# Kernel optimization log

Hardware: AMD Instinct MI355X
Metric: run time of the kernel (lower is better)

The kernel has to match this reference:

```python
import jax, jax.numpy as jnp
import numpy as np

B, T, D = 32, 200, 256
H, DH = 4, 32
INNER = H * DH  # 128
L, FF, NI = 8, 1024, 100000
NB = 64  # gap/recency buckets


def _ln(x, g, b, eps=1e-5):
    m = x.mean(-1, keepdims=True)
    v = jnp.mean((x - m) ** 2, -1, keepdims=True)
    return (x - m) / jnp.sqrt(v + eps) * g + b


def _gelu(x):
    return jax.nn.gelu(x, approximate=False)


def _dwconv_causal(x, w, b):
    # x: [B,T,C], w: [C,k] depthwise kernel, causal left-pad (k-1)
    k = w.shape[1]
    xp = jnp.pad(x, ((0, 0), (k - 1, 0), (0, 0))).transpose(0, 2, 1)  # [B,C,T+k-1]
    out = jax.lax.conv_general_dilated(
        xp, w[:, None, :], (1,), 'VALID',
        dimension_numbers=('NCH', 'OIH', 'NCH'), feature_group_count=w.shape[0])
    return out.transpose(0, 2, 1) + b


def _causal_linear_attention(q, k, v, m4):
    q = (jax.nn.elu(q) + 1.0) * m4
    k = (jax.nn.elu(k) + 1.0) * m4
    v = v * m4
    kv = jnp.einsum('bthd,bthe->bthde', k, v)          # [B,T,H,DH,DH]
    kv_prefix = jnp.cumsum(kv, axis=1)
    k_prefix = jnp.cumsum(k, axis=1)
    num = jnp.einsum('bthd,bthde->bthe', q, kv_prefix)
    den = jnp.sum(q * k_prefix, -1, keepdims=True)
    return num / (den + 1e-6) * m4


def _forward(item_emb, pos_emb, gap_emb, rec_emb, tf_w1, tf_b1, tf_w2, tf_b2,
             in_g, in_b, l_ln1g, l_ln1b, l_win, l_bin, l_wc, l_bc, l_tw, l_tb,
             l_pw, l_pb, l_wmix, l_bmix, l_ln2g, l_ln2b, l_wf1, l_bf1, l_wf2, l_bf2,
             fn_g, fn_b, pg_w, pg_b, uh_w1, uh_b1, uh_lng, uh_lnb, uh_w2, uh_b2,
             item_bias, ids, ts, lens):
    Bb, Tt = ids.shape
    pos = jnp.arange(Tt)
    mask = pos[None, :] >= (Tt - lens)[:, None]  # right-aligned valid mask [B,T]
    prev_ts = jnp.roll(ts, 1, axis=1)
    prev_mask = jnp.roll(mask, 1, axis=1).at[:, 0].set(False)
    zero = jnp.zeros_like(ts)
    gap_vals = jnp.where(mask & prev_mask, jnp.maximum(ts - prev_ts, 0), zero)
    latest = ts[:, -1:]
    rec_vals = jnp.where(mask, jnp.maximum(latest - ts, 0), zero)

    def buck(v, n):
        vf = jnp.maximum(v.astype(jnp.float32), 0.0)
        return jnp.clip(jnp.floor(jnp.log2(vf + 1.0)), 0, n - 1).astype(jnp.int32)

    gb = buck(gap_vals, NB)
    rb = buck(rec_vals, NB)
    rec_raw = jnp.maximum(latest - ts, 0).astype(jnp.float32)
    tf = jnp.stack([jnp.log1p(gb.astype(jnp.float32)), jnp.log1p(rec_raw)], -1)  # [B,T,2]
    dense_time = _gelu(tf @ tf_w1 + tf_b1) @ tf_w2 + tf_b2

    x = item_emb[ids] + pos_emb[None] + gap_emb[gb] + rec_emb[rb] + dense_time
    mf = mask[..., None].astype(x.dtype)
    m4 = mask[..., None, None].astype(x.dtype)
    x = _ln(x, in_g, in_b) * mf

    for i in range(L):
        res = x
        nrm = _ln(x, l_ln1g[i], l_ln1b[i])
        proj = nrm @ l_win[i] + l_bin[i]  # [B,T,D+3*INNER]
        gate = proj[..., :D]
        q = proj[..., D:D + INNER].reshape(Bb, Tt, H, DH)
        k = proj[..., D + INNER:D + 2 * INNER].reshape(Bb, Tt, H, DH)
        v = proj[..., D + 2 * INNER:].reshape(Bb, Tt, H, DH)
        content = _causal_linear_attention(q, k, v, m4).reshape(Bb, Tt, INNER) @ l_wc[i] + l_bc[i]
        temporal = _dwconv_causal(nrm, l_tw[i], l_tb[i])
        positional = _dwconv_causal(nrm, l_pw[i], l_pb[i])
        mixed = jnp.concatenate([content, temporal, positional], -1) @ l_wmix[i] + l_bmix[i]
        x = (res + jax.nn.sigmoid(gate) * mixed) * mf
        h = _ln(x, l_ln2g[i], l_ln2b[i])
        ffn = _gelu(h @ l_wf1[i] + l_bf1[i]) @ l_wf2[i] + l_bf2[i]
        x = (x + ffn) * mf

    x = _ln(x, fn_g, fn_b) * mf
    denom = jnp.maximum(lens, 1)[:, None].astype(x.dtype)
    mean_pooled = (x * mf).sum(1) / denom
    ps = (x @ pg_w + pg_b)[..., 0]
    ps = jnp.where(mask, ps, -1e9)
    pw = jax.nn.softmax(ps, axis=1)[..., None]
    attn_pooled = (pw * x).sum(1)
    last = x[:, -1, :]
    u = jnp.concatenate([last, mean_pooled, attn_pooled], -1)
    u = _gelu(u @ uh_w1 + uh_b1)
    u = _ln(u, uh_lng, uh_lnb)
    u = u @ uh_w2 + uh_b2
    u = u / jnp.maximum(jnp.linalg.norm(u, axis=-1, keepdims=True), 1e-12)
    ie = item_emb[1:]
    ie = ie / jnp.maximum(jnp.linalg.norm(ie, axis=-1, keepdims=True), 1e-12)
    return u @ ie.T + item_bias[1:]


def setup_inputs() -> dict:
    key = jax.random.key(0)
    it = iter(jax.random.split(key, 64))
    def nk():
        return next(it)
    def w(*s):
        return jax.random.normal(nk(), s, jnp.float32) * 0.02
    inp = dict(
        history_ids=jax.random.randint(nk(), (B, T), 0, NI),
        history_timestamps=jnp.sort(jax.random.randint(nk(), (B, T), 0, 1000000), axis=1),
        history_lengths=jax.random.randint(nk(), (B,), 1, T + 1),
        item_emb=w(NI + 1, D).at[0].set(0.0),
        pos_emb=w(T, D), gap_emb=w(NB, D), rec_emb=w(NB, D),
        tf_w1=w(2, D), tf_b1=jnp.zeros((D,)), tf_w2=w(D, D), tf_b2=jnp.zeros((D,)),
        in_g=jnp.ones((D,)), in_b=jnp.zeros((D,)),
        l_ln1g=jnp.ones((L, D)), l_ln1b=jnp.zeros((L, D)),
        l_win=w(L, D, D + 3 * INNER), l_bin=jnp.zeros((L, D + 3 * INNER)),
        l_wc=w(L, INNER, D), l_bc=jnp.zeros((L, D)),
        l_tw=w(L, D, 3), l_tb=jnp.zeros((L, D)),
        l_pw=w(L, D, 5), l_pb=jnp.zeros((L, D)),
        l_wmix=w(L, 3 * D, D), l_bmix=jnp.zeros((L, D)),
        l_ln2g=jnp.ones((L, D)), l_ln2b=jnp.zeros((L, D)),
        l_wf1=w(L, D, FF), l_bf1=jnp.zeros((L, FF)),
        l_wf2=w(L, FF, D), l_bf2=jnp.zeros((L, D)),
        fn_g=jnp.ones((D,)), fn_b=jnp.zeros((D,)),
        pg_w=w(D, 1), pg_b=jnp.zeros((1,)),
        uh_w1=w(3 * D, 1024), uh_b1=jnp.zeros((1024,)),
        uh_lng=jnp.ones((1024,)), uh_lnb=jnp.zeros((1024,)),
        uh_w2=w(1024, D), uh_b2=jnp.zeros((D,)),
        item_bias=jnp.zeros((NI + 1,)),
    )
    return inp


def reference(history_ids, history_timestamps, history_lengths, item_emb, pos_emb,
              gap_emb, rec_emb, tf_w1, tf_b1, tf_w2, tf_b2, in_g, in_b, l_ln1g,
              l_ln1b, l_win, l_bin, l_wc, l_bc, l_tw, l_tb, l_pw, l_pb, l_wmix,
              l_bmix, l_ln2g, l_ln2b, l_wf1, l_bf1, l_wf2, l_bf2, fn_g, fn_b,
              pg_w, pg_b, uh_w1, uh_b1, uh_lng, uh_lnb, uh_w2, uh_b2, item_bias):
    return _forward(item_emb, pos_emb, gap_emb, rec_emb, tf_w1, tf_b1, tf_w2, tf_b2,
                    in_g, in_b, l_ln1g, l_ln1b, l_win, l_bin, l_wc, l_bc, l_tw, l_tb,
                    l_pw, l_pb, l_wmix, l_bmix, l_ln2g, l_ln2b, l_wf1, l_bf1, l_wf2,
                    l_bf2, fn_g, fn_b, pg_w, pg_b, uh_w1, uh_b1, uh_lng, uh_lnb,
                    uh_w2, uh_b2, item_bias, history_ids, history_timestamps,
                    history_lengths)
```

## Files before the change

kernel.cpp:

```cpp
#include <hip/hip_runtime.h>
#include <math.h>

#define B_ 32
#define T_ 200
#define D_ 256
#define H_ 4
#define DH_ 32
#define INNER_ 128
#define L_ 8
#define FF_ 1024
#define NI_ 100000
#define NB_ 64
#define CH_ 25

typedef __attribute__((ext_vector_type(8))) short short8;
typedef __attribute__((ext_vector_type(8))) unsigned short ushort8;
typedef __attribute__((ext_vector_type(4))) unsigned short ushort4v;
typedef __attribute__((ext_vector_type(4))) float floatx4;

__device__ __forceinline__ float gelu_f(float x){
  return 0.5f*x*(1.0f+erff(x*0.70710678118654752f));
}
__device__ __forceinline__ float wsum(float v){
  #pragma unroll
  for (int o=32;o>0;o>>=1) v += __shfl_xor(v,o,64);
  return v;
}
__device__ __forceinline__ unsigned short f2bf(float x){
  unsigned int u = __float_as_uint(x);
  unsigned int r = (u + 0x7fffu + ((u>>16)&1u)) >> 16;
  return (unsigned short)r;
}
__device__ __forceinline__ float bf2f(unsigned short u){
  return __uint_as_float(((unsigned int)u)<<16);
}

__device__ __forceinline__ void cvt_tile(const float* __restrict__ src, unsigned short* __restrict__ dst,
                                         int K, int N, int tk, int tn, int tid, float (*s)[33])
{
  int tx = tid & 31, ty0 = tid >> 5;
  #pragma unroll
  for (int it=0; it<4; ++it){
    int ty = ty0 + it*8;
    s[ty][tx] = src[(size_t)(tk*32+ty)*N + tn*32+tx];
  }
  __syncthreads();
  #pragma unroll
  for (int it=0; it<4; ++it){
    int ty = ty0 + it*8;
    dst[(size_t)(tn*32+ty)*K + tk*32 + tx] = f2bf(s[tx][ty]);
  }
}

__global__ __launch_bounds__(256) void k_cvtAll(
  const float* __restrict__ win, const float* __restrict__ wmix,
  const float* __restrict__ wf1, const float* __restrict__ wf2,
  const float* __restrict__ tfw2, const float* __restrict__ uhw1, const float* __restrict__ uhw2,
  unsigned short* __restrict__ WtPerm, unsigned short* __restrict__ WtMixT,
  unsigned short* __restrict__ WtH)
{
  __shared__ float s[32][33];
  int b = blockIdx.x, tid = threadIdx.x;
  if (b < 6912){
    int l = b / 864, r = b % 864;
    if (r < 160)      cvt_tile(win + (size_t)l*163840, WtPerm + (size_t)l*688128,          256, 640,  r/20,      r%20,      tid, s);
    else if (r < 352){int t=r-160; cvt_tile(wmix + (size_t)l*196608, WtMixT + (size_t)l*196608, 768, 256, t/8, t%8, tid, s);}
    else if (r < 608){int t=r-352; cvt_tile(wf1 + (size_t)l*262144, WtPerm + (size_t)l*688128 + 163840, 256, 1024, t/32, t%32, tid, s);}
    else             {int t=r-608; cvt_tile(wf2 + (size_t)l*262144, WtPerm + (size_t)l*688128 + 425984, 1024, 256, t/8, t%8, tid, s);}
  } else {
    int r = b - 6912;
    if (r < 64)       cvt_tile(tfw2, WtH,        256, 256,  r/8,  r%8,  tid, s);
    else if (r < 832){int t=r-64;  cvt_tile(uhw1, WtH+65536,  768, 1024, t/32, t%32, tid, s);}
    else             {int t=r-832; cvt_tile(uhw2, WtH+851968, 1024, 256, t/8,  t%8,  tid, s);}
  }
}

__global__ __launch_bounds__(256) void k_asm(
  const float* __restrict__ WcombF, const unsigned short* __restrict__ WtMixT,
  unsigned short* __restrict__ WtBig)
{
  int l = blockIdx.x >> 3, g = blockIdx.x & 7;
  int tid = threadIdx.x;
  int n = g*32 + (tid >> 3);
  int k0 = (tid & 7) * 80;
  const float* wc = WcombF + (size_t)l*32768;
  const unsigned short* wm = WtMixT + (size_t)l*196608 + (size_t)n*768;
  unsigned short* dst = WtBig + (size_t)l*163840 + (size_t)n*640;
  for (int kk=0; kk<80; kk++){
    int k = k0 + kk;
    dst[k] = (k < 128) ? f2bf(wc[(size_t)k*256 + n]) : wm[k+128];
  }
}

__global__ __launch_bounds__(256) void k_bfold(
  const float* __restrict__ bc, const float* __restrict__ bmix,
  const float* __restrict__ wmix, float* __restrict__ bmixP)
{
  int l = blockIdx.x; int n = threadIdx.x;
  const float* w = wmix + (size_t)l*196608;
  const float* c = bc + l*256;
  float s = bmix[l*256 + n];
  for (int d=0; d<256; d++) s += c[d]*w[(size_t)d*256 + n];
  bmixP[l*256+n] = s;
}

template<int TN>
__global__ __launch_bounds__(256) void k_gemm_bf(
    const float* __restrict__ A, const unsigned short* __restrict__ Wt,
    const float* __restrict__ bias, float* __restrict__ C,
    int M, int N, int K, int ldA, int ldW, int ldC, int mode,
    size_t sA, size_t sW, size_t sC, size_t sB)
{
  constexpr int NJ = TN/32;
  __shared__ unsigned short Als[128][40];
  __shared__ unsigned short Bls[TN][40];
  int z = blockIdx.z;
  A += (size_t)z*sA; Wt += (size_t)z*sW; C += (size_t)z*sC;
  const float* bz = bias ? bias + (size_t)z*sB : nullptr;
  int tid = threadIdx.x;
  int wave = tid >> 6, lane = tid & 63;
  int wm = (wave >> 1) * 64, wn = (wave & 1) * (TN/2);
  int frow = lane & 15, kg = lane >> 4;
  int bm = blockIdx.y * 128, bn = blockIdx.x * TN;
  int sm = tid >> 1, skh = (tid & 1) * 16;

  floatx4 acc[4][NJ];
  #pragma unroll
  for (int i=0;i<4;i++)
    #pragma unroll
    for (int j=0;j<NJ;j++) acc[i][j] = (floatx4){0.f,0.f,0.f,0.f};

  for (int k0=0; k0<K; k0+=32){
    {
      int gm = bm + sm;
      float f[16];
      if (gm < M){
        const float4* ap = (const float4*)(A + (size_t)gm*ldA + k0 + skh);
        #pragma unroll
        for (int c=0;c<4;c++){ float4 v = ap[c]; f[c*4]=v.x; f[c*4+1]=v.y; f[c*4+2]=v.z; f[c*4+3]=v.w; }
      } else {
        #pragma unroll
        for (int c=0;c<16;c++) f[c]=0.f;
      }
      ushort8 pa, pb;
      #pragma unroll
      for (int c=0;c<8;c++){ pa[c]=f2bf(f[c]); pb[c]=f2bf(f[8+c]); }
      *(ushort8*)&Als[sm][skh]   = pa;
      *(ushort8*)&Als[sm][skh+8] = pb;
    }
    #pragma unroll
    for (int u=0; u<TN/64; u++){
      int li = tid + u*256;
      int row = li >> 2, koff = (li & 3) * 8;
      int gn = bn + row;
      ushort8 wv;
      if (gn < N){
        wv = *(const ushort8*)&Wt[(size_t)gn*ldW + k0 + koff];
      } else {
        for (int c=0;c<8;c++) wv[c]=0;
      }
      *(ushort8*)&Bls[row][koff] = wv;
    }
    __syncthreads();
    short8 af[4], bf[NJ];
    #pragma unroll
    for (int i=0;i<4;i++) af[i] = *(const short8*)&Als[wm + 16*i + frow][kg*8];
    #pragma unroll
    for (int j=0;j<NJ;j++) bf[j] = *(const short8*)&Bls[wn + 16*j + frow][kg*8];
    #pragma unroll
    for (int i=0;i<4;i++)
      #pragma unroll
      for (int j=0;j<NJ;j++)
        acc[i][j] = __builtin_amdgcn_mfma_f32_16x16x32_bf16(af[i], bf[j], acc[i][j], 0, 0, 0);
    __syncthreads();
  }

  #pragma unroll
  for (int j=0;j<NJ;j++){
    int n = bn + wn + 16*j + frow;
    float bv = bz ? bz[n] : 0.f;
    #pragma unroll
    for (int i=0;i<4;i++){
      int m0 = bm + wm + 16*i + kg*4;
      #pragma unroll
      for (int r=0;r<4;r++){
        int m = m0 + r;
        if (m < M){
          float v = acc[i][j][r] + bv;
          if (mode == 1) v = gelu_f(v);
          float* cp = &C[(size_t)m*ldC + n];
          if (mode == 2) v += *cp;
          *cp = v;
        }
      }
    }
  }
}

__global__ __launch_bounds__(256) void k_gemm16(
    const unsigned short* __restrict__ A, const unsigned short* __restrict__ Wt,
    const float* __restrict__ bias, void* __restrict__ Cv,
    int K, int ldA, int ldW, int ldC, int mode)
{
  int tid = threadIdx.x;
  int wave = tid >> 6, lane = tid & 63;
  int frow = lane & 15, kg = lane >> 4;
  int bm = blockIdx.y * 32;
  int bn = blockIdx.x * 128 + wave * 32;

  const unsigned short* a0 = A + (size_t)(bm + frow)*ldA + kg*8;
  const unsigned short* a1 = a0 + (size_t)16*ldA;
  const unsigned short* b0 = Wt + (size_t)(bn + frow)*ldW + kg*8;
  const unsigned short* b1 = b0 + (size_t)16*ldW;

  floatx4 acc[2][2];
  #pragma unroll
  for (int i=0;i<2;i++)
    #pragma unroll
    for (int j=0;j<2;j++) acc[i][j] = (floatx4){0.f,0.f,0.f,0.f};

  #pragma unroll 4
  for (int k0=0; k0<K; k0+=32){
    short8 af0 = *(const short8*)(a0 + k0);
    short8 af1 = *(const short8*)(a1 + k0);
    short8 bf0 = *(const short8*)(b0 + k0);
    short8 bf1 = *(const short8*)(b1 + k0);
    acc[0][0] = __builtin_amdgcn_mfma_f32_16x16x32_bf16(af0, bf0, acc[0][0], 0, 0, 0);
    acc[0][1] = __builtin_amdgcn_mfma_f32_16x16x32_bf16(af0, bf1, acc[0][1], 0, 0, 0);
    acc[1][0] = __builtin_amdgcn_mfma_f32_16x16x32_bf16(af1, bf0, acc[1][0], 0, 0, 0);
    acc[1][1] = __builtin_amdgcn_mfma_f32_16x16x32_bf16(af1, bf1, acc[1][1], 0, 0, 0);
  }

  float* Cf = (float*)Cv;
  unsigned short* Ch = (unsigned short*)Cv;
  #pragma unroll
  for (int j=0;j<2;j++){
    int n = bn + 16*j + frow;
    float bv = bias[n];
    #pragma unroll
    for (int i=0;i<2;i++){
      int m0 = bm + 16*i + kg*4;
      #pragma unroll
      for (int r=0;r<4;r++){
        float v = acc[i][j][r] + bv;
        size_t off = (size_t)(m0+r)*ldC + n;
        if (mode == 1)      Cf[off] = gelu_f(v);
        else if (mode == 2) Cf[off] += v;
        else if (mode == 4) Ch[off] = f2bf(gelu_f(v));
        else                Cf[off] = v;
      }
    }
  }
}

__global__ __launch_bounds__(256) void k_embed(
  const int* __restrict__ ids, const int* __restrict__ ts, const int* __restrict__ lens,
  const float* __restrict__ item_emb, const float* __restrict__ pos_emb,
  const float* __restrict__ gap_emb, const float* __restrict__ rec_emb,
  const float* __restrict__ tf_w1, const float* __restrict__ tf_b1,
  float* __restrict__ xbuf, unsigned short* __restrict__ tfh)
{
  int bt = blockIdx.x;
  int b = bt / T_, t = bt % T_;
  int d = threadIdx.x;
  int len = lens[b];
  int tcur = ts[b*T_+t];
  int tlast = ts[b*T_+T_-1];
  bool mask  = t >= T_ - len;
  bool pmask = (t >= 1) && ((t-1) >= T_ - len);
  int gap = 0;
  if (mask && pmask){ int pv = ts[b*T_+t-1]; gap = max(tcur - pv, 0); }
  int rec = mask ? max(tlast - tcur, 0) : 0;
  int gb = min(max((int)floorf(log2f((float)gap + 1.0f)), 0), NB_-1);
  int rb = min(max((int)floorf(log2f((float)rec + 1.0f)), 0), NB_-1);
  float rec_raw = (float)max(tlast - tcur, 0);
  float tf0 = log1pf((float)gb);
  float tf1 = log1pf(rec_raw);
  float hid = gelu_f(tf0*tf_w1[d] + tf1*tf_w1[D_+d] + tf_b1[d]);
  tfh[(size_t)bt*D_ + d] = f2bf(hid);
  int id = ids[b*T_+t];
  xbuf[(size_t)bt*D_ + d] = item_emb[(size_t)id*D_ + d] + pos_emb[t*D_ + d]
                          + gap_emb[gb*D_ + d] + rec_emb[rb*D_ + d];
}

template<int NC>
__global__ __launch_bounds__(256) void k_ln(
  const float* __restrict__ in, void* __restrict__ out,
  const float* __restrict__ g, const float* __restrict__ bb,
  int rows, const int* __restrict__ lens, int applyMask, int outBf)
{
  int wid = threadIdx.x >> 6, lane = threadIdx.x & 63;
  int r = blockIdx.x*4 + wid;
  if (r >= rows) return;
  const int D = NC*256;
  const float4* rp = (const float4*)(in + (size_t)r*D);
  float4 v[NC];
  float s = 0.f;
  #pragma unroll
  for (int c=0;c<NC;c++){ v[c] = rp[c*64 + lane]; s += v[c].x+v[c].y+v[c].z+v[c].w; }
  s = wsum(s);
  float mean = s / (float)D;
  float q = 0.f;
  #pragma unroll
  for (int c=0;c<NC;c++){
    float a=v[c].x-mean, b2=v[c].y-mean, c2=v[c].z-mean, d2=v[c].w-mean;
    q += a*a + b2*b2 + c2*c2 + d2*d2;
  }
  q = wsum(q);
  float rstd = rsqrtf(q/(float)D + 1e-5f);
  float m = 1.f;
  if (applyMask){ int t = r % T_; int b = r / T_; m = (t >= T_ - lens[b]) ? 1.f : 0.f; }
  #pragma unroll
  for (int c=0;c<NC;c++){
    float4 gg  = ((const float4*)g )[c*64+lane];
    float4 bv  = ((const float4*)bb)[c*64+lane];
    float4 o;
    o.x = ((v[c].x-mean)*rstd*gg.x + bv.x)*m;
    o.y = ((v[c].y-mean)*rstd*gg.y + bv.y)*m;
    o.z = ((v[c].z-mean)*rstd*gg.z + bv.z)*m;
    o.w = ((v[c].w-mean)*rstd*gg.w + bv.w)*m;
    if (outBf){
      ushort4v ob; ob.x=f2bf(o.x); ob.y=f2bf(o.y); ob.z=f2bf(o.z); ob.w=f2bf(o.w);
      ((ushort4v*)((unsigned short*)out + (size_t)r*D))[c*64+lane] = ob;
    } else {
      ((float4*)((float*)out + (size_t)r*D))[c*64+lane] = o;
    }
  }
}

__global__ __launch_bounds__(64) void k_attn_sums(
  const float* __restrict__ proj, const int* __restrict__ lens, float* __restrict__ Ssum)
{
  int blk = blockIdx.x;
  int bh = blk >> 3, c = blk & 7;
  int b = bh >> 2, h = bh & 3;
  int lane = threadIdx.x; int e = lane & 31, half = lane >> 5;
  int tstart = T_ - lens[b];
  __shared__ float sk[CH_*32], sv[CH_*32];
  int t0 = c*CH_;
  for (int idx = lane; idx < CH_*32; idx += 64){
    int tl = idx >> 5, dd = idx & 31;
    int t = t0 + tl;
    float m = (t >= tstart) ? 1.f : 0.f;
    const float* pr = proj + (size_t)(b*T_+t)*640 + h*32 + dd;
    float kw = pr[384], vv = pr[512];
    sk[idx] = (kw > 0.f ? kw + 1.f : __expf(kw)) * m;
    sv[idx] = vv * m;
  }
  __syncthreads();
  float acc[16];
  #pragma unroll
  for (int j=0;j<16;j++) acc[j]=0.f;
  for (int tl=0; tl<CH_; tl++){
    const float4* k4 = (const float4*)(sk + tl*32 + half*16);
    float vf = sv[tl*32 + e];
    #pragma unroll
    for (int jj=0;jj<4;jj++){
      float4 kk = k4[jj];
      acc[jj*4+0] += kk.x*vf;
      acc[jj*4+1] += kk.y*vf;
      acc[jj*4+2] += kk.z*vf;
      acc[jj*4+3] += kk.w*vf;
    }
  }
  float* dst = Ssum + ((size_t)bh*8 + c)*1056;
  #pragma unroll
  for (int j=0;j<16;j++) dst[(half*16+j)*32 + e] = acc[j];
  if (half == 0){
    float s = 0.f;
    for (int tl=0; tl<CH_; tl++) s += sk[tl*32 + e];
    dst[1024 + e] = s;
  }
}

__global__ __launch_bounds__(64) void k_attn_out(
  const float* __restrict__ proj, const int* __restrict__ lens,
  const float* __restrict__ Ssum, unsigned short* __restrict__ cat)
{
  int blk = blockIdx.x;
  int bh = blk >> 3, c = blk & 7;
  int b = bh >> 2, h = bh & 3;
  int lane = threadIdx.x; int e = lane & 31, half = lane >> 5;
  int tstart = T_ - lens[b];
  __shared__ float sq[CH_*32], sk[CH_*32], sv[CH_*32];
  __shared__ float P[1056];
  __shared__ float A[CH_][CH_+1];
  __shared__ float sden[CH_];
  int t0 = c*CH_;
  const float* base = Ssum + (size_t)bh*8*1056;
  for (int idx = lane; idx < 1056; idx += 64){
    float s = 0.f;
    for (int cp=0; cp<c; cp++) s += base[cp*1056 + idx];
    P[idx] = s;
  }
  for (int idx = lane; idx < CH_*32; idx += 64){
    int tl = idx >> 5, dd = idx & 31;
    int t = t0 + tl;
    float m = (t >= tstart) ? 1.f : 0.f;
    const float* pr = proj + (size_t)(b*T_+t)*640 + h*32 + dd;
    float qv = pr[256], kw = pr[384], vv = pr[512];
    sq[idx] = (qv > 0.f ? qv + 1.f : __expf(qv)) * m;
    sk[idx] = (kw > 0.f ? kw + 1.f : __expf(kw)) * m;
    sv[idx] = vv * m;
  }
  __syncthreads();
  for (int idx = lane; idx < CH_*CH_; idx += 64){
    int t = idx / CH_, tp = idx - t*CH_;
    float s = 0.f;
    if (tp <= t){
      const float4* q4 = (const float4*)(sq + t*32);
      const float4* k4 = (const float4*)(sk + tp*32);
      #pragma unroll
      for (int jj=0;jj<8;jj++){
        float4 qq = q4[jj], kk = k4[jj];
        s += qq.x*kk.x + qq.y*kk.y + qq.z*kk.z + qq.w*kk.w;
      }
    }
    A[t][tp] = s;
  }
  __syncthreads();
  if (lane < CH_){
    int t = lane;
    float s = 0.f;
    for (int tp=0; tp<=t; tp++) s += A[t][tp];
    const float* qf = sq + t*32;
    #pragma unroll
    for (int d=0; d<32; d++) s += qf[d]*P[1024+d];
    sden[t] = s;
  }
  __syncthreads();
  int tlo = half ? 13 : 0;
  int thi = half ? CH_ : 13;
  for (int t = tlo; t < thi; t++){
    float num = 0.f;
    for (int tp=0; tp<=t; tp++) num += A[t][tp]*sv[tp*32+e];
    const float* qf = sq + t*32;
    #pragma unroll
    for (int d=0; d<32; d++) num += qf[d]*P[d*32+e];
    int tg = t0 + t;
    float m = (tg >= tstart) ? 1.f : 0.f;
    cat[(size_t)(b*T_+tg)*640 + h*32 + e] = f2bf(num/(sden[t]+1e-6f)*m);
  }
}

__global__ __launch_bounds__(256) void k_dwconv(
  const unsigned short* __restrict__ nrm, const float* __restrict__ tw, const float* __restrict__ tb,
  const float* __restrict__ pw, const float* __restrict__ pb, unsigned short* __restrict__ cat)
{
  int idx = blockIdx.x*256 + threadIdx.x;
  int d = idx & 255; int bt = idx >> 8; int t = bt % T_;
  float xs[5];
  #pragma unroll
  for (int j=0;j<5;j++){
    int tt = t - 4 + j;
    xs[j] = (tt >= 0) ? bf2f(nrm[(size_t)(bt - 4 + j)*D_ + d]) : 0.f;
  }
  float tmp = tw[d*3+0]*xs[2] + tw[d*3+1]*xs[3] + tw[d*3+2]*xs[4] + tb[d];
  float pos = pb[d];
  #pragma unroll
  for (int j=0;j<5;j++) pos += pw[d*5+j]*xs[j];
  cat[(size_t)bt*640 + 128 + d] = f2bf(tmp);
  cat[(size_t)bt*640 + 384 + d] = f2bf(pos);
}

__global__ __launch_bounds__(256) void k_postmix_ln(
  float* __restrict__ x, const float* __restrict__ proj, const float* __restrict__ mixed,
  const int* __restrict__ lens, const float* __restrict__ g, const float* __restrict__ bb,
  unsigned short* __restrict__ h)
{
  int wid = threadIdx.x >> 6, lane = threadIdx.x & 63;
  int r = blockIdx.x*4 + wid;
  int t = r % T_, b = r / T_;
  float m = (t >= T_ - lens[b]) ? 1.f : 0.f;
  float4 xv = ((const float4*)(x     + (size_t)r*256))[lane];
  float4 gv = ((const float4*)(proj  + (size_t)r*640))[lane];
  float4 mx = ((const float4*)(mixed + (size_t)r*256))[lane];
  float4 xn;
  xn.x = (xv.x + mx.x/(1.f+__expf(-gv.x)))*m;
  xn.y = (xv.y + mx.y/(1.f+__expf(-gv.y)))*m;
  xn.z = (xv.z + mx.z/(1.f+__expf(-gv.z)))*m;
  xn.w = (xv.w + mx.w/(1.f+__expf(-gv.w)))*m;
  float s = wsum(xn.x+xn.y+xn.z+xn.w);
  float mean = s/256.f;
  float a=xn.x-mean, b2=xn.y-mean, c2=xn.z-mean, d2=xn.w-mean;
  float q = wsum(a*a+b2*b2+c2*c2+d2*d2);
  float rstd = rsqrtf(q/256.f + 1e-5f);
  ((float4*)(x + (size_t)r*256))[lane] = xn;
  float4 gg = ((const float4*)g )[lane];
  float4 bv = ((const float4*)bb)[lane];
  ushort4v o;
  o.x = f2bf(a*rstd*gg.x + bv.x);
  o.y = f2bf(b2*rstd*gg.y + bv.y);
  o.z = f2bf(c2*rstd*gg.z + bv.z);
  o.w = f2bf(d2*rstd*gg.w + bv.w);
  ((ushort4v*)(h + (size_t)r*256))[lane] = o;
}

__global__ __launch_bounds__(256) void k_addln(
  float* __restrict__ x, const float* __restrict__ f, const int* __restrict__ lens,
  const float* __restrict__ g, const float* __restrict__ bb,
  unsigned short* __restrict__ nrm, int maskLN)
{
  int wid = threadIdx.x >> 6, lane = threadIdx.x & 63;
  int r = blockIdx.x*4 + wid;
  int t = r % T_, b = r / T_;
  float m = (t >= T_ - lens[b]) ? 1.f : 0.f;
  float4 xv = ((const float4*)(x + (size_t)r*256))[lane];
  float4 fv = ((const float4*)(f + (size_t)r*256))[lane];
  float4 xn;
  xn.x = (xv.x + fv.x)*m;
  xn.y = (xv.y + fv.y)*m;
  xn.z = (xv.z + fv.z)*m;
  xn.w = (xv.w + fv.w)*m;
  float s = wsum(xn.x+xn.y+xn.z+xn.w);
  float mean = s/256.f;
  float a=xn.x-mean, b2=xn.y-mean, c2=xn.z-mean, d2=xn.w-mean;
  float q = wsum(a*a+b2*b2+c2*c2+d2*d2);
  float rstd = rsqrtf(q/256.f + 1e-5f);
  ((float4*)(x + (size_t)r*256))[lane] = xn;
  float ml = maskLN ? m : 1.f;
  float4 gg = ((const float4*)g )[lane];
  float4 bv = ((const float4*)bb)[lane];
  ushort4v o;
  o.x = f2bf((a*rstd*gg.x + bv.x)*ml);
  o.y = f2bf((b2*rstd*gg.y + bv.y)*ml);
  o.z = f2bf((c2*rstd*gg.z + bv.z)*ml);
  o.w = f2bf((d2*rstd*gg.w + bv.w)*ml);
  ((ushort4v*)(nrm + (size_t)r*256))[lane] = o;
}

__global__ __launch_bounds__(256) void k_pool(
  const unsigned short* __restrict__ x, const int* __restrict__ lens,
  const float* __restrict__ pg_w, const float* __restrict__ pg_b,
  float* __restrict__ u0)
{
  int b = blockIdx.x;
  int tid = threadIdx.x, wid = tid>>6, lane = tid&63;
  __shared__ float sps[T_];
  __shared__ float spw[T_];
  int len = lens[b]; int tstart = T_ - len;
  const float4* pw4 = (const float4*)pg_w;
  float4 wv = pw4[lane];
  for (int t = wid; t < T_; t += 4){
    ushort4v xv = ((const ushort4v*)(x + (size_t)(b*T_+t)*D_))[lane];
    float dot = bf2f(xv.x)*wv.x + bf2f(xv.y)*wv.y + bf2f(xv.z)*wv.z + bf2f(xv.w)*wv.w;
    dot = wsum(dot);
    if (lane==0) sps[t] = (t >= tstart) ? dot + pg_b[0] : -1e9f;
  }
  __syncthreads();
  float mx = -1e30f;
  for (int t=0;t<T_;t++) mx = fmaxf(mx, sps[t]);
  float sum = 0.f;
  for (int t=0;t<T_;t++) sum += __expf(sps[t]-mx);
  float inv = 1.f/sum;
  if (tid < T_) spw[tid] = __expf(sps[tid]-mx)*inv;
  __syncthreads();
  int d = tid;
  float macc=0.f, aacc=0.f;
  for (int t=0;t<T_;t++){
    float v = bf2f(x[(size_t)(b*T_+t)*D_ + d]);
    macc += v;
    aacc += spw[t]*v;
  }
  u0[b*768 + d]       = bf2f(x[(size_t)(b*T_+T_-1)*D_ + d]);
  u0[b*768 + 256 + d] = macc / (float)max(len,1);
  u0[b*768 + 512 + d] = aacc;
}

__global__ __launch_bounds__(64) void k_norm(float* __restrict__ u, unsigned short* __restrict__ ub)
{
  int b = blockIdx.x; int lane = threadIdx.x;
  float4* r = (float4*)(u + b*256);
  float4 v = r[lane];
  float ss = v.x*v.x + v.y*v.y + v.z*v.z + v.w*v.w;
  ss = wsum(ss);
  float sc = 1.f/fmaxf(sqrtf(ss), 1e-12f);
  v.x*=sc; v.y*=sc; v.z*=sc; v.w*=sc;
  r[lane]=v;
  ub[b*256 + lane*4 + 0] = f2bf(v.x);
  ub[b*256 + lane*4 + 1] = f2bf(v.y);
  ub[b*256 + lane*4 + 2] = f2bf(v.z);
  ub[b*256 + lane*4 + 3] = f2bf(v.w);
}

__global__ __launch_bounds__(256) void k_score2(
  const float* __restrict__ item_emb, const unsigned short* __restrict__ ub,
  const float* __restrict__ item_bias, float* __restrict__ out)
{
  int tid = threadIdx.x;
  int wave = tid >> 6, lane = tid & 63;
  int frow = lane & 15, kg = lane >> 4;
  int n0 = blockIdx.x * 128 + wave * 32;

  int g0 = n0 + frow, g1 = n0 + 16 + frow;
  bool ok0 = g0 < NI_, ok1 = g1 < NI_;
  const float* ip0 = item_emb + (size_t)(g0+1)*256 + kg*8;
  const float* ip1 = item_emb + (size_t)(g1+1)*256 + kg*8;
  const unsigned short* up0 = ub + frow*256 + kg*8;
  const unsigned short* up1 = up0 + 16*256;

  floatx4 acc[2][2];
  #pragma unroll
  for (int i=0;i<2;i++)
    #pragma unroll
    for (int j=0;j<2;j++) acc[i][j] = (floatx4){0.f,0.f,0.f,0.f};
  float ss0 = 0.f, ss1 = 0.f;

  #pragma unroll
  for (int k0=0; k0<256; k0+=32){
    float4 a0, a1, c0, c1;
    if (ok0){ a0 = *(const float4*)(ip0 + k0); a1 = *(const float4*)(ip0 + k0 + 4); }
    else    { a0 = (float4){0,0,0,0}; a1 = a0; }
    if (ok1){ c0 = *(const float4*)(ip1 + k0); c1 = *(const float4*)(ip1 + k0 + 4); }
    else    { c0 = (float4){0,0,0,0}; c1 = c0; }
    ss0 += a0.x*a0.x + a0.y*a0.y + a0.z*a0.z + a0.w*a0.w
         + a1.x*a1.x + a1.y*a1.y + a1.z*a1.z + a1.w*a1.w;
    ss1 += c0.x*c0.x + c0.y*c0.y + c0.z*c0.z + c0.w*c0.w
         + c1.x*c1.x + c1.y*c1.y + c1.z*c1.z + c1.w*c1.w;
    short8 af0, af1;
    af0[0]=(short)f2bf(a0.x); af0[1]=(short)f2bf(a0.y); af0[2]=(short)f2bf(a0.z); af0[3]=(short)f2bf(a0.w);
    af0[4]=(short)f2bf(a1.x); af0[5]=(short)f2bf(a1.y); af0[6]=(short)f2bf(a1.z); af0[7]=(short)f2bf(a1.w);
    af1[0]=(short)f2bf(c0.x); af1[1]=(short)f2bf(c0.y); af1[2]=(short)f2bf(c0.z); af1[3]=(short)f2bf(c0.w);
    af1[4]=(short)f2bf(c1.x); af1[5]=(short)f2bf(c1.y); af1[6]=(short)f2bf(c1.z); af1[7]=(short)f2bf(c1.w);
    short8 bf0 = *(const short8*)(up0 + k0);
    short8 bf1 = *(const short8*)(up1 + k0);
    acc[0][0] = __builtin_amdgcn_mfma_f32_16x16x32_bf16(af0, bf0, acc[0][0], 0, 0, 0);
    acc[0][1] = __builtin_amdgcn_mfma_f32_16x16x32_bf16(af0, bf1, acc[0][1], 0, 0, 0);
    acc[1][0] = __builtin_amdgcn_mfma_f32_16x16x32_bf16(af1, bf0, acc[1][0], 0, 0, 0);
    acc[1][1] = __builtin_amdgcn_mfma_f32_16x16x32_bf16(af1, bf1, acc[1][1], 0, 0, 0);
  }

  ss0 += __shfl_xor(ss0, 16, 64); ss0 += __shfl_xor(ss0, 32, 64);
  ss1 += __shfl_xor(ss1, 16, 64); ss1 += __shfl_xor(ss1, 32, 64);

  #pragma unroll
  for (int i=0;i<2;i++){
    int nb = n0 + 16*i + kg*4;
    if (nb >= NI_) continue;
    float ssr = i ? ss1 : ss0;
    float sc[4], bv[4];
    #pragma unroll
    for (int r=0;r<4;r++){
      float ssv = __shfl(ssr, kg*4 + r, 64);
      sc[r] = 1.f/fmaxf(sqrtf(ssv), 1e-12f);
      bv[r] = item_bias[nb + r + 1];
    }
    #pragma unroll
    for (int j=0;j<2;j++){
      int row = 16*j + frow;
      float4 o;
      o.x = acc[i][j][0]*sc[0] + bv[0];
      o.y = acc[i][j][1]*sc[1] + bv[1];
      o.z = acc[i][j][2]*sc[2] + bv[2];
      o.w = acc[i][j][3]*sc[3] + bv[3];
      *(float4*)&out[(size_t)row*NI_ + nb] = o;
    }
  }
}

extern "C" void kernel_launch(void* const* d_in, const int* in_sizes, int n_in,
                              void* d_out, int out_size, void* d_ws, size_t ws_size,
                              hipStream_t stream)
{
  const int* ids  = (const int*)d_in[0];
  const int* ts   = (const int*)d_in[1];
  const int* lens = (const int*)d_in[2];
  const float* item_emb = (const float*)d_in[3];
  const float* pos_emb  = (const float*)d_in[4];
  const float* gap_emb  = (const float*)d_in[5];
  const float* rec_emb  = (const float*)d_in[6];
  const float* tf_w1 = (const float*)d_in[7];
  const float* tf_b1 = (const float*)d_in[8];
  const float* tf_w2 = (const float*)d_in[9];
  const float* tf_b2 = (const float*)d_in[10];
  const float* in_g  = (const float*)d_in[11];
  const float* in_b  = (const float*)d_in[12];
  const float* l_ln1g = (const float*)d_in[13];
  const float* l_ln1b = (const float*)d_in[14];
  const float* l_win  = (const float*)d_in[15];
  const float* l_bin  = (const float*)d_in[16];
  const float* l_wc   = (const float*)d_in[17];
  const float* l_bc   = (const float*)d_in[18];
  const float* l_tw   = (const float*)d_in[19];
  const float* l_tb   = (const float*)d_in[20];
  const float* l_pw   = (const float*)d_in[21];
  const float* l_pb   = (const float*)d_in[22];
  const float* l_wmix = (const float*)d_in[23];
  const float* l_bmix = (const float*)d_in[24];
  const float* l_ln2g = (const float*)d_in[25];
  const float* l_ln2b = (const float*)d_in[26];
  const float* l_wf1  = (const float*)d_in[27];
  const float* l_bf1  = (const float*)d_in[28];
  const float* l_wf2  = (const float*)d_in[29];
  const float* l_bf2  = (const float*)d_in[30];
  const float* fn_g = (const float*)d_in[31];
  const float* fn_b = (const float*)d_in[32];
  const float* pg_w = (const float*)d_in[33];
  const float* pg_b = (const float*)d_in[34];
  const float* uh_w1 = (const float*)d_in[35];
  const float* uh_b1 = (const float*)d_in[36];
  const float* uh_lng = (const float*)d_in[37];
  const float* uh_lnb = (const float*)d_in[38];
  const float* uh_w2 = (const float*)d_in[39];
  const float* uh_b2 = (const float*)d_in[40];
  const float* item_bias = (const float*)d_in[41];
  float* out = (float*)d_out;

  const int MT = B_*T_;
  float* ws   = (float*)d_ws;
  float* xbuf = ws;
  float* tmp  = xbuf + (size_t)MT*D_;
  float* proj = tmp  + (size_t)MT*D_;
  float* cat  = proj + (size_t)MT*640;
  float* mid  = cat  + (size_t)MT*640;
  float* u0   = mid  + (size_t)MT*FF_;
  float* u1   = u0 + 32*768;
  float* u2   = u1 + 32*1024;
  float* WcombF = u2 + 32*256;
  float* bmixP  = WcombF + 262144;
  float* Ssum   = bmixP + 2048;
  unsigned short* WtPerm = (unsigned short*)(Ssum + 1081344);
  unsigned short* WtMixT = WtPerm + 5505024;
  unsigned short* WtBig  = WtMixT + 1572864;
  unsigned short* WtH    = WtBig  + 1310720;
  unsigned short* u2b    = WtH    + 1114112;

  unsigned short* tmpb = (unsigned short*)tmp;
  unsigned short* catb = (unsigned short*)cat;
  unsigned short* midb = (unsigned short*)(mid + (size_t)MT*D_);

  k_cvtAll<<<8000, 256, 0, stream>>>(l_win, l_wmix, l_wf1, l_wf2, tf_w2, uh_w1, uh_w2,
                                     WtPerm, WtMixT, WtH);
  k_gemm_bf<64><<<dim3(4,1,8), 256, 0, stream>>>(l_wc, WtMixT, nullptr, WcombF,
                                                 128, 256, 256, 256, 768, 256, 0,
                                                 (size_t)128*256, (size_t)196608, (size_t)32768, 0);
  k_asm<<<64, 256, 0, stream>>>(WcombF, WtMixT, WtBig);
  k_bfold<<<8, 256, 0, stream>>>(l_bc, l_bmix, l_wmix, bmixP);

  k_embed<<<MT, 256, 0, stream>>>(ids, ts, lens, item_emb, pos_emb, gap_emb, rec_emb,
                                  tf_w1, tf_b1, xbuf, tmpb);
  k_gemm16<<<dim3(2,200), 256, 0, stream>>>(tmpb, WtH, tf_b2, xbuf, 256, 256, 256, 256, 2);
  k_ln<1><<<MT/4, 256, 0, stream>>>(xbuf, xbuf, in_g, in_b, MT, lens, 1, 0);
  k_ln<1><<<MT/4, 256, 0, stream>>>(xbuf, tmpb, l_ln1g, l_ln1b, MT, lens, 0, 1);

  for (int i=0;i<L_;i++){
    const unsigned short* WL = WtPerm + (size_t)i*688128;
    k_gemm16<<<dim3(5,200), 256, 0, stream>>>(tmpb, WL, l_bin+i*640, proj, 256, 256, 256, 640, 0);
    k_attn_sums<<<B_*H_*8, 64, 0, stream>>>(proj, lens, Ssum);
    k_attn_out<<<B_*H_*8, 64, 0, stream>>>(proj, lens, Ssum, catb);
    k_dwconv<<<MT, 256, 0, stream>>>(tmpb, l_tw+i*768, l_tb+i*256, l_pw+i*1280, l_pb+i*256, catb);
    k_gemm16<<<dim3(2,200), 256, 0, stream>>>(catb, WtBig+(size_t)i*163840, bmixP+i*256, mid,
                                              640, 640, 640, 256, 0);
    k_postmix_ln<<<MT/4, 256, 0, stream>>>(xbuf, proj, mid, lens, l_ln2g+i*256, l_ln2b+i*256, tmpb);
    k_gemm16<<<dim3(8,200), 256, 0, stream>>>(tmpb, WL+163840, l_bf1+i*FF_, midb,
                                              256, 256, 256, FF_, 4);
    k_gemm16<<<dim3(2,200), 256, 0, stream>>>(midb, WL+425984, l_bf2+i*256, proj,
                                              1024, 1024, 1024, 256, 0);
    bool last = (i == L_-1);
    k_addln<<<MT/4, 256, 0, stream>>>(xbuf, proj, lens,
                                      last ? fn_g : l_ln1g+(i+1)*256,
                                      last ? fn_b : l_ln1b+(i+1)*256,
                                      tmpb, last ? 1 : 0);
  }

  k_pool<<<B_, 256, 0, stream>>>(tmpb, lens, pg_w, pg_b, u0);
  k_gemm_bf<128><<<dim3(8,1), 256, 0, stream>>>(u0, WtH+65536, uh_b1, u1,
                                                32, 1024, 768, 768, 768, 1024, 1, 0,0,0,0);
  k_ln<4><<<8, 256, 0, stream>>>(u1, u1, uh_lng, uh_lnb, 32, lens, 0, 0);
  k_gemm_bf<64><<<dim3(4,1), 256, 0, stream>>>(u1, WtH+851968, uh_b2, u2,
                                               32, 256, 1024, 1024, 1024, 256, 0, 0,0,0,0);
  k_norm<<<B_, 64, 0, stream>>>(u2, u2b);

  k_score2<<<(NI_+127)/128, 256, 0, stream>>>(item_emb, u2b, item_bias, out);
}
```

Baseline: 1.949 ms.

## Template GEMM on K, fuse LN pair, fold prefix scan into dwconv kernel

Makes the K dimension of the MFMA GEMM a template parameter so the k-loop fully unrolls. Fuses the two back-to-back layernorms at the input into one kernel. Replaces the per-block O(c) prefix accumulation of chunk sums in attention with an in-place prefix scan, run as extra blocks of the depthwise-conv kernel, so each attention block reads one precomputed prefix. Attention output blocks go from 64 to 128 threads. Full unrolling at K=1024 may raise register pressure and code size.

Result: faster. 1.721 ms (-11.7%).

```diff
diff --git a/kernel.cpp b/kernel.cpp
--- a/kernel.cpp
+++ b/kernel.cpp
@@ -197,10 +197,11 @@
   }
 }
 
+template<int K>
 __global__ __launch_bounds__(256) void k_gemm16(
     const unsigned short* __restrict__ A, const unsigned short* __restrict__ Wt,
     const float* __restrict__ bias, void* __restrict__ Cv,
-    int K, int ldA, int ldW, int ldC, int mode)
+    int ldA, int ldW, int ldC, int mode)
 {
   int tid = threadIdx.x;
   int wave = tid >> 6, lane = tid & 63;
@@ -219,7 +220,7 @@
     #pragma unroll
     for (int j=0;j<2;j++) acc[i][j] = (floatx4){0.f,0.f,0.f,0.f};
 
-  #pragma unroll 4
+  #pragma unroll
   for (int k0=0; k0<K; k0+=32){
     short8 af0 = *(const short8*)(a0 + k0);
     short8 af1 = *(const short8*)(a1 + k0);
@@ -328,6 +329,45 @@
   }
 }
 
+__global__ __launch_bounds__(256) void k_lnln(
+  float* __restrict__ x, const int* __restrict__ lens,
+  const float* __restrict__ g1, const float* __restrict__ b1,
+  const float* __restrict__ g2, const float* __restrict__ b2,
+  unsigned short* __restrict__ nrm)
+{
+  int wid = threadIdx.x >> 6, lane = threadIdx.x & 63;
+  int r = blockIdx.x*4 + wid;
+  int t = r % T_, b = r / T_;
+  float m = (t >= T_ - lens[b]) ? 1.f : 0.f;
+  float4 v = ((const float4*)(x + (size_t)r*256))[lane];
+  float s = wsum(v.x+v.y+v.z+v.w);
+  float mean = s/256.f;
+  float a=v.x-mean, b2v=v.y-mean, c2=v.z-mean, d2=v.w-mean;
+  float q = wsum(a*a+b2v*b2v+c2*c2+d2*d2);
+  float rstd = rsqrtf(q/256.f + 1e-5f);
+  float4 gg = ((const float4*)g1)[lane];
+  float4 bv = ((const float4*)b1)[lane];
+  float4 xn;
+  xn.x = (a*rstd*gg.x + bv.x)*m;
+  xn.y = (b2v*rstd*gg.y + bv.y)*m;
+  xn.z = (c2*rstd*gg.z + bv.z)*m;
+  xn.w = (d2*rstd*gg.w + bv.w)*m;
+  ((float4*)(x + (size_t)r*256))[lane] = xn;
+  float s2 = wsum(xn.x+xn.y+xn.z+xn.w);
+  float mean2 = s2/256.f;
+  float a2=xn.x-mean2, b22=xn.y-mean2, c22=xn.z-mean2, d22=xn.w-mean2;
+  float q2 = wsum(a2*a2+b22*b22+c22*c22+d22*d22);
+  float rstd2 = rsqrtf(q2/256.f + 1e-5f);
+  float4 gg2 = ((const float4*)g2)[lane];
+  float4 bv2 = ((const float4*)b2)[lane];
+  ushort4v o;
+  o.x = f2bf(a2*rstd2*gg2.x + bv2.x);
+  o.y = f2bf(b22*rstd2*gg2.y + bv2.y);
+  o.z = f2bf(c22*rstd2*gg2.z + bv2.z);
+  o.w = f2bf(d22*rstd2*gg2.w + bv2.w);
+  ((ushort4v*)(nrm + (size_t)r*256))[lane] = o;
+}
+
 __global__ __launch_bounds__(64) void k_attn_sums(
   const float* __restrict__ proj, const int* __restrict__ lens, float* __restrict__ Ssum)
 {
@@ -373,27 +413,58 @@
   }
 }
 
-__global__ __launch_bounds__(64) void k_attn_out(
+__global__ __launch_bounds__(256) void k_dwpfx(
+  const unsigned short* __restrict__ nrm, const float* __restrict__ tw, const float* __restrict__ tb,
+  const float* __restrict__ pw, const float* __restrict__ pb, unsigned short* __restrict__ cat,
+  float* __restrict__ Ssum)
+{
+  int bid = blockIdx.x;
+  if (bid < 6400){
+    int idx = bid*256 + threadIdx.x;
+    int d = idx & 255; int bt = idx >> 8; int t = bt % T_;
+    float xs[5];
+    #pragma unroll
+    for (int j=0;j<5;j++){
+      int tt = t - 4 + j;
+      xs[j] = (tt >= 0) ? bf2f(nrm[(size_t)(bt - 4 + j)*D_ + d]) : 0.f;
+    }
+    float tmp = tw[d*3+0]*xs[2] + tw[d*3+1]*xs[3] + tw[d*3+2]*xs[4] + tb[d];
+    float pos = pb[d];
+    #pragma unroll
+    for (int j=0;j<5;j++) pos += pw[d*5+j]*xs[j];
+    cat[(size_t)bt*640 + 128 + d] = f2bf(tmp);
+    cat[(size_t)bt*640 + 384 + d] = f2bf(pos);
+  } else {
+    int idx = (bid - 6400)*256 + threadIdx.x;
+    int bh = idx / 1056, r = idx - bh*1056;
+    float* p = Ssum + (size_t)bh*8*1056 + r;
+    float s = p[0];
+    #pragma unroll
+    for (int c=1;c<8;c++){ s += p[(size_t)c*1056]; p[(size_t)c*1056] = s; }
+  }
+}
+
+__global__ __launch_bounds__(128) void k_attn_out(
   const float* __restrict__ proj, const int* __restrict__ lens,
   const float* __restrict__ Ssum, unsigned short* __restrict__ cat)
 {
   int blk = blockIdx.x;
   int bh = blk >> 3, c = blk & 7;
   int b = bh >> 2, h = bh & 3;
-  int lane = threadIdx.x; int e = lane & 31, half = lane >> 5;
+  int tid = threadIdx.x; int e = tid & 31, qg = tid >> 5;
   int tstart = T_ - lens[b];
   __shared__ float sq[CH_*32], sk[CH_*32], sv[CH_*32];
   __shared__ float P[1056];
   __shared__ float A[CH_][CH_+1];
   __shared__ float sden[CH_];
   int t0 = c*CH_;
-  const float* base = Ssum + (size_t)bh*8*1056;
-  for (int idx = lane; idx < 1056; idx += 64){
-    float s = 0.f;
-    for (int cp=0; cp<c; cp++) s += base[cp*1056 + idx];
-    P[idx] = s;
-  }
-  for (int idx = lane; idx < CH_*32; idx += 64){
+  if (c > 0){
+    const float* Pp = Ssum + ((size_t)bh*8 + (c-1))*1056;
+    for (int idx = tid; idx < 1056; idx += 128) P[idx] = Pp[idx];
+  } else {
+    for (int idx = tid; idx < 1056; idx += 128) P[idx] = 0.f;
+  }
+  for (int idx = tid; idx < CH_*32; idx += 128){
     int tl = idx >> 5, dd = idx & 31;
     int t = t0 + tl;
     float m = (t >= tstart) ? 1.f : 0.f;
@@ -404,7 +475,7 @@
     sv[idx] = vv * m;
   }
   __syncthreads();
-  for (int idx = lane; idx < CH_*CH_; idx += 64){
+  for (int idx = tid; idx < CH_*CH_; idx += 128){
     int t = idx / CH_, tp = idx - t*CH_;
     float s = 0.f;
     if (tp <= t){
@@ -419,8 +490,8 @@
     A[t][tp] = s;
   }
   __syncthreads();
-  if (lane < CH_){
-    int t = lane;
+  if (tid < CH_){
+    int t = tid;
     float s = 0.f;
     for (int tp=0; tp<=t; tp++) s += A[t][tp];
     const float* qf = sq + t*32;
@@ -429,8 +500,7 @@
     sden[t] = s;
   }
   __syncthreads();
-  int tlo = half ? 13 : 0;
-  int thi = half ? CH_ : 13;
+  int tlo = (qg*CH_) >> 2, thi = ((qg+1)*CH_) >> 2;
   for (int t = tlo; t < thi; t++){
     float num = 0.f;
     for (int tp=0; tp<=t; tp++) num += A[t][tp]*sv[tp*32+e];
@@ -441,26 +511,6 @@
     float m = (tg >= tstart) ? 1.f : 0.f;
     cat[(size_t)(b*T_+tg)*640 + h*32 + e] = f2bf(num/(sden[t]+1e-6f)*m);
   }
-}
-
-__global__ __launch_bounds__(256) void k_dwconv(
-  const unsigned short* __restrict__ nrm, const float* __restrict__ tw, const float* __restrict__ tb,
-  const float* __restrict__ pw, const float* __restrict__ pb, unsigned short* __restrict__ cat)
-{
-  int idx = blockIdx.x*256 + threadIdx.x;
-  int d = idx & 255; int bt = idx >> 8; int t = bt % T_;
-  float xs[5];
-  #pragma unroll
-  for (int j=0;j<5;j++){
-    int tt = t - 4 + j;
-    xs[j] = (tt >= 0) ? bf2f(nrm[(size_t)(bt - 4 + j)*D_ + d]) : 0.f;
-  }
-  float tmp = tw[d*3+0]*xs[2] + tw[d*3+1]*xs[3] + tw[d*3+2]*xs[4] + tb[d];
-  float pos = pb[d];
-  #pragma unroll
-  for (int j=0;j<5;j++) pos += pw[d*5+j]*xs[j];
-  cat[(size_t)bt*640 + 128 + d] = f2bf(tmp);
-  cat[(size_t)bt*640 + 384 + d] = f2bf(pos);
 }
 
 __global__ __launch_bounds__(256) void k_postmix_ln(
@@ -739,23 +789,23 @@
 
   k_embed<<<MT, 256, 0, stream>>>(ids, ts, lens, item_emb, pos_emb, gap_emb, rec_emb,
                                   tf_w1, tf_b1, xbuf, tmpb);
-  k_gemm16<<<dim3(2,200), 256, 0, stream>>>(tmpb, WtH, tf_b2, xbuf, 256, 256, 256, 256, 2);
-  k_ln<1><<<MT/4, 256, 0, stream>>>(xbuf, xbuf, in_g, in_b, MT, lens, 1, 0);
-  k_ln<1><<<MT/4, 256, 0, stream>>>(xbuf, tmpb, l_ln1g, l_ln1b, MT, lens, 0, 1);
+  k_gemm16<256><<<dim3(2,200), 256, 0, stream>>>(tmpb, WtH, tf_b2, xbuf, 256, 256, 256, 2);
+  k_lnln<<<MT/4, 256, 0, stream>>>(xbuf, lens, in_g, in_b, l_ln1g, l_ln1b, tmpb);
 
   for (int i=0;i<L_;i++){
     const unsigned short* WL = WtPerm + (size_t)i*688128;
-    k_gemm16<<<dim3(5,200), 256, 0, stream>>>(tmpb, WL, l_bin+i*640, proj, 256, 256, 256, 640, 0);
+    k_gemm16<256><<<dim3(5,200), 256, 0, stream>>>(tmpb, WL, l_bin+i*640, proj, 256, 256, 640, 0);
     k_attn_sums<<<B_*H_*8, 64, 0, stream>>>(proj, lens, Ssum);
-    k_attn_out<<<B_*H_*8, 64, 0, stream>>>(proj, lens, Ssum, catb);
-    k_dwconv<<<MT, 256, 0, stream>>>(tmpb, l_tw+i*768, l_tb+i*256, l_pw+i*1280, l_pb+i*256, catb);
-    k_gemm16<<<dim3(2,200), 256, 0, stream>>>(catb, WtBig+(size_t)i*163840, bmixP+i*256, mid,
-                                              640, 640, 640, 256, 0);
+    k_dwpfx<<<6928, 256, 0, stream>>>(tmpb, l_tw+i*768, l_tb+i*256, l_pw+i*1280, l_pb+i*256,
+                                      catb, Ssum);
+    k_attn_out<<<B_*H_*8, 128, 0, stream>>>(proj, lens, Ssum, catb);
+    k_gemm16<640><<<dim3(2,200), 256, 0, stream>>>(catb, WtBig+(size_t)i*163840, bmixP+i*256, mid,
+                                                   640, 640, 256, 0);
     k_postmix_ln<<<MT/4, 256, 0, stream>>>(xbuf, proj, mid, lens, l_ln2g+i*256, l_ln2b+i*256, tmpb);
-    k_gemm16<<<dim3(8,200), 256, 0, stream>>>(tmpb, WL+163840, l_bf1+i*FF_, midb,
-                                              256, 256, 256, FF_, 4);
-    k_gemm16<<<dim3(2,200), 256, 0, stream>>>(midb, WL+425984, l_bf2+i*256, proj,
-                                              1024, 1024, 1024, 256, 0);
+    k_gemm16<256><<<dim3(8,200), 256, 0, stream>>>(tmpb, WL+163840, l_bf1+i*FF_, midb,
+                                                   256, 256, FF_, 4);
+    k_gemm16<1024><<<dim3(2,200), 256, 0, stream>>>(midb, WL+425984, l_bf2+i*256, proj,
+                                                    1024, 1024, 256, 0);
     bool last = (i == L_-1);
     k_addln<<<MT/4, 256, 0, stream>>>(xbuf, proj, lens,
                                       last ? fn_g : l_ln1g+(i+1)*256,
```
